# Optimization experiments

Hardware: AMD Instinct MI355X
Metric: run time of the kernel (lower is better)

## Reference

```python
import jax, jax.numpy as jnp
import numpy as np

N = 50000
E = 800000
D_IN = 256
D_HID = 256
D_OUT = 256
EPS = 1e-5


def _sage_conv(x, src, dst, Wl, Wr, b, n_nodes):
    # mean aggregation of source-node features at target nodes (PyG SAGEConv default)
    msg = x[src]                                              # [E, d_in]
    agg = jax.ops.segment_sum(msg, dst, num_segments=n_nodes)  # [N, d_in]
    deg = jax.ops.segment_sum(jnp.ones((src.shape[0],), x.dtype), dst,
                              num_segments=n_nodes)           # [N]
    agg = agg / jnp.maximum(deg, 1.0)[:, None]
    return agg @ Wl + x @ Wr + b


def _bn(h, gamma, beta, mean, var):
    # inference-mode BatchNorm1d
    return (h - mean) * jax.lax.rsqrt(var + EPS) * gamma + beta


def setup_inputs() -> dict:
    key = jax.random.key(0)
    ks = jax.random.split(key, 16)
    x = jax.random.normal(ks[0], (N, D_IN), dtype=jnp.float32)
    edge_index = jax.random.randint(ks[1], (2, E), 0, N, dtype=jnp.int32)

    def lin(k, din, dout):
        return jax.random.normal(k, (din, dout), dtype=jnp.float32) / np.sqrt(din)

    inp = {"x": x, "edge_index": edge_index}
    dims = [(D_IN, D_HID), (D_HID, D_HID), (D_HID, D_OUT)]
    ki = 2
    for i, (din, dout) in enumerate(dims):
        inp[f"Wl{i}"] = lin(ks[ki], din, dout); ki += 1
        inp[f"Wr{i}"] = lin(ks[ki], din, dout); ki += 1
        inp[f"b{i}"] = jnp.zeros((dout,), jnp.float32)
    for i in range(2):
        inp[f"gamma{i}"] = jnp.ones((D_HID,), jnp.float32)
        inp[f"beta{i}"] = jnp.zeros((D_HID,), jnp.float32)
        inp[f"mean{i}"] = jax.random.normal(ks[ki], (D_HID,), jnp.float32) * 0.1; ki += 1
        inp[f"var{i}"] = jnp.ones((D_HID,), jnp.float32) + 0.1 * jax.random.uniform(ks[ki], (D_HID,)); ki += 1
    return inp


def reference(x, edge_index, Wl0, Wr0, b0, Wl1, Wr1, b1, Wl2, Wr2, b2,
              gamma0, beta0, mean0, var0, gamma1, beta1, mean1, var1):
    src, dst = edge_index[0], edge_index[1]
    h = x
    layers = [(Wl0, Wr0, b0, gamma0, beta0, mean0, var0),
              (Wl1, Wr1, b1, gamma1, beta1, mean1, var1)]
    for Wl, Wr, b, g, bt, m, v in layers:
        h_res = h
        h = _sage_conv(h, src, dst, Wl, Wr, b, N)
        h = jax.nn.relu(_bn(h, g, bt, m, v))
        # dropout is identity in eval mode
        if h_res.shape[1] == h.shape[1]:
            h = h + h_res
    return _sage_conv(h, src, dst, Wl2, Wr2, b2, N)
```

## Files before the change

kernel.cpp:

```cpp
#include <hip/hip_runtime.h>
#include <hip/hip_bf16.h>

#define NN 50000
#define NE 800000
#define DD 256
#define EPSV 1e-5f

typedef float f32x4 __attribute__((ext_vector_type(4)));
typedef short bf16x8s __attribute__((ext_vector_type(8)));
typedef unsigned int uint32;
typedef uint32 u32x4 __attribute__((ext_vector_type(4)));

__device__ __forceinline__ float bf2f(unsigned int u16v) {
  return __builtin_bit_cast(float, u16v << 16);
}
__device__ __forceinline__ unsigned short f2bf(float f) {
  return __builtin_bit_cast(unsigned short, __float2bfloat16(f));
}
__device__ __forceinline__ void mfma_bf16(bf16x8s a, bf16x8s b, f32x4& c) {
  asm("v_mfma_f32_16x16x32_bf16 %0, %1, %2, %0" : "+v"(c) : "v"(a), "v"(b));
}
__device__ __forceinline__ void gload_lds16(const void* g, void* l) {
  __builtin_amdgcn_global_load_lds((const __attribute__((address_space(1))) void*)g,
                                   (__attribute__((address_space(3))) void*)l, 16, 0, 0);
}



__global__ void deg_count_k(const int* __restrict__ ei, int* __restrict__ deg) {
  int e = blockIdx.x * 256 + threadIdx.x;
  if (e < NE) atomicAdd(&deg[ei[NE + e]], 1);
}

__global__ void scan1_k(const int* __restrict__ deg, int* __restrict__ row_ptr,
                        int* __restrict__ blockSums) {
  __shared__ int s[1024];
  int gid = blockIdx.x * 1024 + threadIdx.x;
  int v = (gid < NN) ? deg[gid] : 0;
  s[threadIdx.x] = v;
  __syncthreads();
  for (int off = 1; off < 1024; off <<= 1) {
    int t = (threadIdx.x >= off) ? s[threadIdx.x - off] : 0;
    __syncthreads();
    s[threadIdx.x] += t;
    __syncthreads();
  }
  if (gid < NN) row_ptr[gid] = s[threadIdx.x] - v;
  if (threadIdx.x == 1023) blockSums[blockIdx.x] = s[1023];
}

__global__ void scan2_k(const int* __restrict__ blockSums, int* __restrict__ blockOffs,
                        int* __restrict__ row_ptr, int nblocks) {
  if (threadIdx.x == 0) {
    int run = 0;
    for (int i = 0; i < nblocks; ++i) { blockOffs[i] = run; run += blockSums[i]; }
    row_ptr[NN] = run;
  }
}

__global__ void scan3_k(int* __restrict__ row_ptr, const int* __restrict__ blockOffs,
                        const int* __restrict__ deg, float* __restrict__ deg_inv,
                        int* __restrict__ cursor) {
  int gid = blockIdx.x * 1024 + threadIdx.x;
  if (gid < NN) {
    int v = row_ptr[gid] + blockOffs[blockIdx.x];
    row_ptr[gid] = v;
    cursor[gid] = v;
    deg_inv[gid] = 1.0f / (float)max(deg[gid], 1);
  }
}

__global__ void csr_fill_k(const int* __restrict__ ei, int* __restrict__ cursor,
                           unsigned short* __restrict__ col16) {
  int e = blockIdx.x * 256 + threadIdx.x;
  if (e < NE) {
    int pos = atomicAdd(&cursor[ei[NE + e]], 1);
    col16[pos] = (unsigned short)ei[e];
  }
}


__global__ __launch_bounds__(256) void prep_k(
    const float* __restrict__ x,
    const float* __restrict__ W0, const float* __restrict__ W1,
    const float* __restrict__ W2, const float* __restrict__ W3,
    const float* __restrict__ W4, const float* __restrict__ W5,
    float* __restrict__ xF, unsigned short* __restrict__ wt) {
  if (blockIdx.x < 3125) {
    int unit = blockIdx.x * 256 + threadIdx.x;
    int c = unit / NN, node = unit - c * NN;
    const float4* src = reinterpret_cast<const float4*>(x + (size_t)node * DD + c * 16);
    float4* dst = reinterpret_cast<float4*>(xF + (size_t)unit * 16);
#pragma unroll
    for (int i = 0; i < 4; ++i) dst[i] = src[i];
  } else {
    int bb = blockIdx.x - 3125;
    int p = bb >> 6;
    const float* W = (p == 0) ? W0 : (p == 1) ? W1 : (p == 2) ? W2
                     : (p == 3) ? W3 : (p == 4) ? W4 : W5;
    unsigned short* thi = wt + (size_t)(2 * p) * 65536;
    unsigned short* tlo = wt + (size_t)(2 * p + 1) * 65536;
    int gid = (bb & 63) * 256 + threadIdx.x;
    int n = gid >> 6, k4 = (gid & 63) << 2;
    ushort4 hi, lo;
    unsigned short* hp = &hi.x; unsigned short* lp = &lo.x;
#pragma unroll
    for (int r = 0; r < 4; ++r) {
      float v = W[(size_t)(k4 + r) * DD + n];
      unsigned short h = f2bf(v);
      hp[r] = h;
      lp[r] = f2bf(v - bf2f(h));
    }
    *reinterpret_cast<ushort4*>(thi + (size_t)n * DD + k4) = hi;
    *reinterpret_cast<ushort4*>(tlo + (size_t)n * DD + k4) = lo;
  }
}


__global__ __launch_bounds__(256) void sage_agg_k(
    const float* __restrict__ act, const int* __restrict__ rp,
    const unsigned short* __restrict__ ci, const float* __restrict__ deg_inv,
    float* __restrict__ agg) {
  int b = blockIdx.x;
  int ph = (b >= 6256);
  int bb = ph ? b - 6256 : b;
  int c = ph * 8 + (bb & 7);
  int grp = bb >> 3;
  int node = grp * 64 + (threadIdx.x >> 2);
  if (node >= NN) return;
  int q4 = (threadIdx.x & 3) * 4;

  const float* base = act + (size_t)c * NN * 16;
  int beg = rp[node], end = rp[node + 1];

  f32x4 a0 = (f32x4)0.f, a1 = (f32x4)0.f;
  int e = beg;
  for (; e + 2 <= end; e += 2) {
    int s0 = (int)ci[e], s1 = (int)ci[e + 1];
    f32x4 v0 = *reinterpret_cast<const f32x4*>(base + (size_t)s0 * 16 + q4);
    f32x4 v1 = *reinterpret_cast<const f32x4*>(base + (size_t)s1 * 16 + q4);
    a0 += v0;
    a1 += v1;
  }
  if (e < end)
    a0 += *reinterpret_cast<const f32x4*>(base + (size_t)ci[e] * 16 + q4);
  a0 += a1;
  float di = deg_inv[node];
  a0 *= di;
  *reinterpret_cast<f32x4*>(agg + ((size_t)c * NN + node) * 16 + q4) = a0;
}


template <bool DO_BN>
__global__ __launch_bounds__(512) void sage_gemm_k(
    const float* __restrict__ aggF, const float* __restrict__ hF,
    const unsigned short* __restrict__ wlHi, const unsigned short* __restrict__ wlLo,
    const unsigned short* __restrict__ wrHi, const unsigned short* __restrict__ wrLo,
    const float* __restrict__ bias,
    const float* __restrict__ gamma, const float* __restrict__ beta,
    const float* __restrict__ mean, const float* __restrict__ var,
    float* __restrict__ outF, float* __restrict__ outC) {
  __shared__ __attribute__((aligned(128))) char lds[40960];

  int tid = threadIdx.x, wave = tid >> 6, l = tid & 63;
  int lr = l & 15, lq = l >> 4;
  int sub = wave & 3, h = wave >> 2;
  int m0 = blockIdx.x * 64;

  f32x4 acc[8];
#pragma unroll
  for (int j = 0; j < 8; ++j) acc[j] = (f32x4)0.f;

#pragma unroll 1
  for (int t = 0; t < 16; ++t) {
    bool first = t < 8;
    const float* Ap = first ? aggF : hF;
    int t7 = t & 7;
#pragma unroll
    for (int i = 0; i < 5; ++i) {
      int u = wave * 5 + i;
      if (u < 8) {
        int row = m0 + (u & 3) * 16 + (l & 15);
        row = row < NN ? row : NN - 1;
        gload_lds16(Ap + ((size_t)(2 * t7 + (u >> 2)) * NN + row) * 16 + (l >> 4) * 4,
                    &lds[u * 1024 + l * 16]);
      } else {
        int ub = u - 8, j = ub >> 1, p = ub & 1;
        const unsigned short* W = first ? (p ? wlLo : wlHi) : (p ? wrLo : wrHi);
        gload_lds16(W + (size_t)(j * 16 + (l & 15)) * DD + t7 * 32 + (l >> 4) * 8,
                    &lds[8192 + ub * 1024 + l * 16]);
      }
    }
    __syncthreads();
    int ua = (lq >> 1) * 4 + sub;
    int abase = ua * 1024 + (lq & 1) * 512 + lr * 16;
    f32x4 f0 = *reinterpret_cast<const f32x4*>(&lds[abase]);
    f32x4 f1 = *reinterpret_cast<const f32x4*>(&lds[abase + 256]);
    float af[8] = {f0[0], f0[1], f0[2], f0[3], f1[0], f1[1], f1[2], f1[3]};
    u32x4 hw, lw;
#pragma unroll
    for (int i = 0; i < 4; ++i) {
      uint32 b0 = __builtin_bit_cast(uint32, af[2 * i]);
      uint32 b1 = __builtin_bit_cast(uint32, af[2 * i + 1]);
      hw[i] = (b1 & 0xffff0000u) | (b0 >> 16);
      float l0 = af[2 * i] - __builtin_bit_cast(float, b0 & 0xffff0000u);
      float l1 = af[2 * i + 1] - __builtin_bit_cast(float, b1 & 0xffff0000u);
      lw[i] = (uint32)f2bf(l0) | ((uint32)f2bf(l1) << 16);
    }
    bf16x8s aH = __builtin_bit_cast(bf16x8s, hw);
    bf16x8s aL = __builtin_bit_cast(bf16x8s, lw);
#pragma unroll
    for (int jj = 0; jj < 8; ++jj) {
      int j = h * 8 + jj;
      bf16x8s bH = *reinterpret_cast<const bf16x8s*>(&lds[8192 + (j * 2 + 0) * 1024 + l * 16]);
      bf16x8s bL = *reinterpret_cast<const bf16x8s*>(&lds[8192 + (j * 2 + 1) * 1024 + l * 16]);
      mfma_bf16(aH, bH, acc[jj]);
      mfma_bf16(aH, bL, acc[jj]);
      mfma_bf16(aL, bH, acc[jj]);
    }
    __syncthreads();
  }

#pragma unroll
  for (int jj = 0; jj < 8; ++jj) {
    int cj = h * 8 + jj;
    int n = cj * 16 + lr;
    float bb = bias[n], sc = 0.f, sh = 0.f;
    if (DO_BN) {
      float s = gamma[n] * rsqrtf(var[n] + EPSV);
      sc = s;
      sh = beta[n] - mean[n] * s;
    }
#pragma unroll
    for (int reg = 0; reg < 4; ++reg) {
      int m = m0 + sub * 16 + lq * 4 + reg;
      if (m < NN) {
        float v = acc[jj][reg] + bb;
        if (DO_BN) {
          size_t ui = ((size_t)cj * NN + m) * 16 + lr;
          v = fmaxf(v * sc + sh, 0.f) + hF[ui];
          outC[ui] = v;
        } else {
          outF[(size_t)m * DD + n] = v;
        }
      }
    }
  }
}


extern "C" void kernel_launch(void* const* d_in, const int* in_sizes, int n_in,
                              void* d_out, int out_size, void* d_ws, size_t ws_size,
                              hipStream_t stream) {
  const float* x   = (const float*)d_in[0];
  const int*   ei  = (const int*)d_in[1];
  const float* Wl[3] = {(const float*)d_in[2], (const float*)d_in[5], (const float*)d_in[8]};
  const float* Wr[3] = {(const float*)d_in[3], (const float*)d_in[6], (const float*)d_in[9]};
  const float* bs[3] = {(const float*)d_in[4], (const float*)d_in[7], (const float*)d_in[10]};
  const float* g0  = (const float*)d_in[11];
  const float* be0 = (const float*)d_in[12];
  const float* mu0 = (const float*)d_in[13];
  const float* va0 = (const float*)d_in[14];
  const float* g1  = (const float*)d_in[15];
  const float* be1 = (const float*)d_in[16];
  const float* mu1 = (const float*)d_in[17];
  const float* va1 = (const float*)d_in[18];
  float* out = (float*)d_out;

  char* w = (char*)d_ws;
  const size_t o_deg    = 0;
  const size_t o_rowptr = 262144;
  const size_t o_cursor = 524288;
  const size_t o_col16  = 786432;
  const size_t o_deginv = 2621440;
  const size_t o_bsum   = 2883584;
  const size_t o_boff   = 2887680;
  const size_t o_wt     = 2891776;
  const size_t ACT      = (size_t)16 * NN * 64;
  const size_t o_xF     = 6291456;
  const size_t o_h1F    = o_xF + ACT;
  const size_t o_aggF   = o_xF + 2 * ACT;

  int*   deg     = (int*)(w + o_deg);
  int*   row_ptr = (int*)(w + o_rowptr);
  int*   cursor  = (int*)(w + o_cursor);
  unsigned short* col16 = (unsigned short*)(w + o_col16);
  float* deg_inv = (float*)(w + o_deginv);
  int*   bsum    = (int*)(w + o_bsum);
  int*   boff    = (int*)(w + o_boff);
  unsigned short* wt = (unsigned short*)(w + o_wt);
  float* xF   = (float*)(w + o_xF);
  float* h1F  = (float*)(w + o_h1F);
  float* aggF = (float*)(w + o_aggF);

  unsigned short* wlT[3][2];
  unsigned short* wrT[3][2];
  for (int l = 0; l < 3; ++l) {
    wlT[l][0] = wt + (size_t)(4 * l + 0) * 65536;
    wlT[l][1] = wt + (size_t)(4 * l + 1) * 65536;
    wrT[l][0] = wt + (size_t)(4 * l + 2) * 65536;
    wrT[l][1] = wt + (size_t)(4 * l + 3) * 65536;
  }

  const int SCAN_BLOCKS = (NN + 1023) / 1024;

  hipMemsetAsync(deg, 0, NN * sizeof(int), stream);
  deg_count_k<<<NE / 256, 256, 0, stream>>>(ei, deg);
  scan1_k<<<SCAN_BLOCKS, 1024, 0, stream>>>(deg, row_ptr, bsum);
  scan2_k<<<1, 64, 0, stream>>>(bsum, boff, row_ptr, SCAN_BLOCKS);
  scan3_k<<<SCAN_BLOCKS, 1024, 0, stream>>>(row_ptr, boff, deg, deg_inv, cursor);
  csr_fill_k<<<NE / 256, 256, 0, stream>>>(ei, cursor, col16);

  prep_k<<<3509, 256, 0, stream>>>(x, Wl[0], Wr[0], Wl[1], Wr[1], Wl[2], Wr[2], xF, wt);

  const int AGRID = 12512;
  dim3 ggrid((NN + 63) / 64);

  sage_agg_k<<<AGRID, 256, 0, stream>>>(xF, row_ptr, col16, deg_inv, aggF);
  sage_gemm_k<true><<<ggrid, 512, 0, stream>>>(
      aggF, xF, wlT[0][0], wlT[0][1], wrT[0][0], wrT[0][1],
      bs[0], g0, be0, mu0, va0, nullptr, h1F);
  sage_agg_k<<<AGRID, 256, 0, stream>>>(h1F, row_ptr, col16, deg_inv, aggF);
  sage_gemm_k<true><<<ggrid, 512, 0, stream>>>(
      aggF, h1F, wlT[1][0], wlT[1][1], wrT[1][0], wrT[1][1],
      bs[1], g1, be1, mu1, va1, nullptr, xF);
  sage_agg_k<<<AGRID, 256, 0, stream>>>(xF, row_ptr, col16, deg_inv, aggF);
  sage_gemm_k<false><<<ggrid, 512, 0, stream>>>(
      aggF, xF, wlT[2][0], wlT[2][1], wrT[2][0], wrT[2][1],
      bs[2], nullptr, nullptr, nullptr, nullptr, out, nullptr);
}
```

Baseline: 749.5 us.

## Degree-sort nodes for aggregation, unroll gather by 4, double-buffer GEMM LDS

Builds a per-degree histogram and a node permutation so aggregation waves process nodes with similar degree together, which reduces divergence in the per-node gather loop. The gather loop is unrolled to four independent accumulators to keep more loads in flight. The GEMM kernel gets two LDS buffers so the next K-tile's global-to-LDS loads are issued before computing the current one. The costs are extra preprocessing kernels and atomics, output writes that are no longer coalesced across nodes, and doubled LDS (80 KB) that may lower GEMM occupancy.

```diff
diff --git a/kernel.cpp b/kernel.cpp
--- a/kernel.cpp
+++ b/kernel.cpp
@@ -60,13 +60,31 @@
 
 __global__ void scan3_k(int* __restrict__ row_ptr, const int* __restrict__ blockOffs,
                         const int* __restrict__ deg, float* __restrict__ deg_inv,
-                        int* __restrict__ cursor) {
+                        int* __restrict__ cursor, int* __restrict__ dh) {
   int gid = blockIdx.x * 1024 + threadIdx.x;
   if (gid < NN) {
     int v = row_ptr[gid] + blockOffs[blockIdx.x];
     row_ptr[gid] = v;
     cursor[gid] = v;
-    deg_inv[gid] = 1.0f / (float)max(deg[gid], 1);
+    int d = deg[gid];
+    deg_inv[gid] = 1.0f / (float)max(d, 1);
+    atomicAdd(&dh[min(d, 63)], 1);
+  }
+}
+
+__global__ void dscan_k(const int* __restrict__ dh, int* __restrict__ dcur) {
+  if (threadIdx.x == 0) {
+    int run = 0;
+    for (int i = 0; i < 64; ++i) { dcur[i] = run; run += dh[i]; }
+  }
+}
+
+__global__ void dperm_k(const int* __restrict__ deg, int* __restrict__ dcur,
+                        int* __restrict__ nperm) {
+  int gid = blockIdx.x * 256 + threadIdx.x;
+  if (gid < NN) {
+    int pos = atomicAdd(&dcur[min(deg[gid], 63)], 1);
+    nperm[pos] = gid;
   }
 }
 
@@ -120,31 +138,31 @@
 __global__ __launch_bounds__(256) void sage_agg_k(
     const float* __restrict__ act, const int* __restrict__ rp,
     const unsigned short* __restrict__ ci, const float* __restrict__ deg_inv,
-    float* __restrict__ agg) {
+    const int* __restrict__ nperm, float* __restrict__ agg) {
   int b = blockIdx.x;
   int ph = (b >= 6256);
   int bb = ph ? b - 6256 : b;
   int c = ph * 8 + (bb & 7);
-  int grp = bb >> 3;
-  int node = grp * 64 + (threadIdx.x >> 2);
-  if (node >= NN) return;
+  int slot = (bb >> 3) * 64 + (threadIdx.x >> 2);
+  if (slot >= NN) return;
+  int node = nperm[slot];
   int q4 = (threadIdx.x & 3) * 4;
 
   const float* base = act + (size_t)c * NN * 16;
   int beg = rp[node], end = rp[node + 1];
 
-  f32x4 a0 = (f32x4)0.f, a1 = (f32x4)0.f;
+  f32x4 a0 = (f32x4)0.f, a1 = (f32x4)0.f, a2 = (f32x4)0.f, a3 = (f32x4)0.f;
   int e = beg;
-  for (; e + 2 <= end; e += 2) {
-    int s0 = (int)ci[e], s1 = (int)ci[e + 1];
-    f32x4 v0 = *reinterpret_cast<const f32x4*>(base + (size_t)s0 * 16 + q4);
-    f32x4 v1 = *reinterpret_cast<const f32x4*>(base + (size_t)s1 * 16 + q4);
-    a0 += v0;
-    a1 += v1;
-  }
-  if (e < end)
+  for (; e + 4 <= end; e += 4) {
+    int s0 = (int)ci[e], s1 = (int)ci[e + 1], s2 = (int)ci[e + 2], s3 = (int)ci[e + 3];
+    a0 += *reinterpret_cast<const f32x4*>(base + (size_t)s0 * 16 + q4);
+    a1 += *reinterpret_cast<const f32x4*>(base + (size_t)s1 * 16 + q4);
+    a2 += *reinterpret_cast<const f32x4*>(base + (size_t)s2 * 16 + q4);
+    a3 += *reinterpret_cast<const f32x4*>(base + (size_t)s3 * 16 + q4);
+  }
+  for (; e < end; ++e)
     a0 += *reinterpret_cast<const f32x4*>(base + (size_t)ci[e] * 16 + q4);
-  a0 += a1;
+  a0 = (a0 + a1) + (a2 + a3);
   float di = deg_inv[node];
   a0 *= di;
   *reinterpret_cast<f32x4*>(agg + ((size_t)c * NN + node) * 16 + q4) = a0;
@@ -160,7 +178,7 @@
     const float* __restrict__ gamma, const float* __restrict__ beta,
     const float* __restrict__ mean, const float* __restrict__ var,
     float* __restrict__ outF, float* __restrict__ outC) {
-  __shared__ __attribute__((aligned(128))) char lds[40960];
+  __shared__ __attribute__((aligned(128))) char lds[2][40960];
 
   int tid = threadIdx.x, wave = tid >> 6, l = tid & 63;
   int lr = l & 15, lq = l >> 4;
@@ -171,8 +189,7 @@
 #pragma unroll
   for (int j = 0; j < 8; ++j) acc[j] = (f32x4)0.f;
 
-#pragma unroll 1
-  for (int t = 0; t < 16; ++t) {
+  auto STAGE = [&](char* L, int t) {
     bool first = t < 8;
     const float* Ap = first ? aggF : hF;
     int t7 = t & 7;
@@ -180,22 +197,24 @@
     for (int i = 0; i < 5; ++i) {
       int u = wave * 5 + i;
       if (u < 8) {
-        int row = m0 + (u & 3) * 16 + (l & 15);
+        int row = m0 + (u & 3) * 16 + lr;
         row = row < NN ? row : NN - 1;
-        gload_lds16(Ap + ((size_t)(2 * t7 + (u >> 2)) * NN + row) * 16 + (l >> 4) * 4,
-                    &lds[u * 1024 + l * 16]);
+        gload_lds16(Ap + ((size_t)(2 * t7 + (u >> 2)) * NN + row) * 16 + lq * 4,
+                    L + u * 1024 + l * 16);
       } else {
         int ub = u - 8, j = ub >> 1, p = ub & 1;
         const unsigned short* W = first ? (p ? wlLo : wlHi) : (p ? wrLo : wrHi);
-        gload_lds16(W + (size_t)(j * 16 + (l & 15)) * DD + t7 * 32 + (l >> 4) * 8,
-                    &lds[8192 + ub * 1024 + l * 16]);
+        gload_lds16(W + (size_t)(j * 16 + lr) * DD + t7 * 32 + lq * 8,
+                    L + 8192 + ub * 1024 + l * 16);
       }
     }
-    __syncthreads();
+  };
+
+  auto COMPUTE = [&](const char* L) {
     int ua = (lq >> 1) * 4 + sub;
     int abase = ua * 1024 + (lq & 1) * 512 + lr * 16;
-    f32x4 f0 = *reinterpret_cast<const f32x4*>(&lds[abase]);
-    f32x4 f1 = *reinterpret_cast<const f32x4*>(&lds[abase + 256]);
+    f32x4 f0 = *reinterpret_cast<const f32x4*>(&L[abase]);
+    f32x4 f1 = *reinterpret_cast<const f32x4*>(&L[abase + 256]);
     float af[8] = {f0[0], f0[1], f0[2], f0[3], f1[0], f1[1], f1[2], f1[3]};
     u32x4 hw, lw;
 #pragma unroll
@@ -212,12 +231,20 @@
 #pragma unroll
     for (int jj = 0; jj < 8; ++jj) {
       int j = h * 8 + jj;
-      bf16x8s bH = *reinterpret_cast<const bf16x8s*>(&lds[8192 + (j * 2 + 0) * 1024 + l * 16]);
-      bf16x8s bL = *reinterpret_cast<const bf16x8s*>(&lds[8192 + (j * 2 + 1) * 1024 + l * 16]);
+      bf16x8s bH = *reinterpret_cast<const bf16x8s*>(&L[8192 + (j * 2 + 0) * 1024 + l * 16]);
+      bf16x8s bL = *reinterpret_cast<const bf16x8s*>(&L[8192 + (j * 2 + 1) * 1024 + l * 16]);
       mfma_bf16(aH, bH, acc[jj]);
       mfma_bf16(aH, bL, acc[jj]);
       mfma_bf16(aL, bH, acc[jj]);
     }
+  };
+
+  STAGE(lds[0], 0);
+  __syncthreads();
+#pragma unroll 1
+  for (int t = 0; t < 16; ++t) {
+    if (t < 15) STAGE(lds[(t + 1) & 1], t + 1);
+    COMPUTE(lds[t & 1]);
     __syncthreads();
   }
 
@@ -269,25 +296,31 @@
 
   char* w = (char*)d_ws;
   const size_t o_deg    = 0;
+  const size_t o_dh     = 204800;
+  const size_t o_dcur   = 205056;
   const size_t o_rowptr = 262144;
   const size_t o_cursor = 524288;
   const size_t o_col16  = 786432;
   const size_t o_deginv = 2621440;
   const size_t o_bsum   = 2883584;
   const size_t o_boff   = 2887680;
-  const size_t o_wt     = 2891776;
+  const size_t o_nperm  = 2891776;
+  const size_t o_wt     = 3145728;
   const size_t ACT      = (size_t)16 * NN * 64;
   const size_t o_xF     = 6291456;
   const size_t o_h1F    = o_xF + ACT;
   const size_t o_aggF   = o_xF + 2 * ACT;
 
   int*   deg     = (int*)(w + o_deg);
+  int*   dh      = (int*)(w + o_dh);
+  int*   dcur    = (int*)(w + o_dcur);
   int*   row_ptr = (int*)(w + o_rowptr);
   int*   cursor  = (int*)(w + o_cursor);
   unsigned short* col16 = (unsigned short*)(w + o_col16);
   float* deg_inv = (float*)(w + o_deginv);
   int*   bsum    = (int*)(w + o_bsum);
   int*   boff    = (int*)(w + o_boff);
+  int*   nperm   = (int*)(w + o_nperm);
   unsigned short* wt = (unsigned short*)(w + o_wt);
   float* xF   = (float*)(w + o_xF);
   float* h1F  = (float*)(w + o_h1F);
@@ -304,11 +337,13 @@
 
   const int SCAN_BLOCKS = (NN + 1023) / 1024;
 
-  hipMemsetAsync(deg, 0, NN * sizeof(int), stream);
+  hipMemsetAsync(w, 0, 205312, stream);
   deg_count_k<<<NE / 256, 256, 0, stream>>>(ei, deg);
   scan1_k<<<SCAN_BLOCKS, 1024, 0, stream>>>(deg, row_ptr, bsum);
   scan2_k<<<1, 64, 0, stream>>>(bsum, boff, row_ptr, SCAN_BLOCKS);
-  scan3_k<<<SCAN_BLOCKS, 1024, 0, stream>>>(row_ptr, boff, deg, deg_inv, cursor);
+  scan3_k<<<SCAN_BLOCKS, 1024, 0, stream>>>(row_ptr, boff, deg, deg_inv, cursor, dh);
+  dscan_k<<<1, 64, 0, stream>>>(dh, dcur);
+  dperm_k<<<(NN + 255) / 256, 256, 0, stream>>>(deg, dcur, nperm);
   csr_fill_k<<<NE / 256, 256, 0, stream>>>(ei, cursor, col16);
 
   prep_k<<<3509, 256, 0, stream>>>(x, Wl[0], Wr[0], Wl[1], Wr[1], Wl[2], Wr[2], xF, wt);
@@ -316,15 +351,15 @@
   const int AGRID = 12512;
   dim3 ggrid((NN + 63) / 64);
 
-  sage_agg_k<<<AGRID, 256, 0, stream>>>(xF, row_ptr, col16, deg_inv, aggF);
+  sage_agg_k<<<AGRID, 256, 0, stream>>>(xF, row_ptr, col16, deg_inv, nperm, aggF);
   sage_gemm_k<true><<<ggrid, 512, 0, stream>>>(
       aggF, xF, wlT[0][0], wlT[0][1], wrT[0][0], wrT[0][1],
       bs[0], g0, be0, mu0, va0, nullptr, h1F);
-  sage_agg_k<<<AGRID, 256, 0, stream>>>(h1F, row_ptr, col16, deg_inv, aggF);
+  sage_agg_k<<<AGRID, 256, 0, stream>>>(h1F, row_ptr, col16, deg_inv, nperm, aggF);
   sage_gemm_k<true><<<ggrid, 512, 0, stream>>>(
       aggF, h1F, wlT[1][0], wlT[1][1], wrT[1][0], wrT[1][1],
       bs[1], g1, be1, mu1, va1, nullptr, xF);
-  sage_agg_k<<<AGRID, 256, 0, stream>>>(xF, row_ptr, col16, deg_inv, aggF);
+  sage_agg_k<<<AGRID, 256, 0, stream>>>(xF, row_ptr, col16, deg_inv, nperm, aggF);
   sage_gemm_k<false><<<ggrid, 512, 0, stream>>>(
       aggF, xF, wlT[2][0], wlT[2][1], wrT[2][0], wrT[2][1],
       bs[2], nullptr, nullptr, nullptr, nullptr, out, nullptr);
```

After: 1.487 ms. 1.98x slower.
